# Optimization experiments

Measured on AMD Instinct MI355X. Metric: run time of the kernel, lower is better.

The kernel has to match this reference:

```python
import jax, jax.numpy as jnp
import numpy as np

B, NX, NY, NZ = 2, 64, 64, 64
D, CI, CO, F = 3, 32, 32, 64  # spatial dims, chan in/out, n_modes


def setup_inputs() -> dict:
    key = jax.random.key(0)
    ka, kx, ky, k1, k2, k3, k4, k5, k6 = jax.random.split(key, 9)
    omega, c = 30.0 / 300.0, 6.0
    u = lambda k, shape, scale: scale * (2.0 * jax.random.uniform(k, shape, jnp.float32) - 1.0)
    return {
        "a": jax.random.normal(ka, (B, NX, NY, NZ, CI), jnp.float32),
        "x": jax.random.uniform(kx, (B, NX, NY, NZ, D), jnp.float32),
        "y": jax.random.uniform(ky, (B, NX, NY, NZ, D), jnp.float32),
        "modes_a": u(k1, (F, CI), np.sqrt(c / (CI + F))),
        "modes_x": u(k2, (F, D), np.sqrt(c / (D + F)) * omega),
        "modes_y": u(k3, (F, D), np.sqrt(c / (D + F)) * omega),
        "modes_u": u(k4, (F, CO), np.sqrt(c / (F + CO))),
        "fc_w": jax.random.normal(k5, (CI, CO), jnp.float32) / np.sqrt(CI),
        "fc_b": jax.random.normal(k6, (CO,), jnp.float32) * 0.01,
    }


def reference(a, x, y, modes_a, modes_x, modes_y, modes_u, fc_w, fc_b):
    # SpectralAttention: Fourier-feature linear attention.
    # NOTE: source forward passes x for both coordinate args (att(h, x, x)).
    A = jnp.einsum('bxyzi,fi->bxyzf', a, modes_a)                       # [B,NX,NY,NZ,F]
    X = jnp.exp(-2j * np.pi * jnp.einsum('bxyzd,gd->bxyzg', x, modes_x))  # complex64
    Y = jnp.exp(2j * np.pi * jnp.einsum('bxyzd,gd->bxyzg', x, modes_y))   # complex64
    N = x.shape[1] * x.shape[2] * x.shape[3]
    AX = jnp.einsum('bxyzf,bxyzg->bfg', A.astype(X.dtype), X)           # [B,F,F] complex
    U = jnp.einsum('bfg,bxyzg->bxyzf', AX, Y).real / N                  # [B,NX,NY,NZ,F]
    u = jnp.einsum('bxyzf,fo->bxyzo', U, modes_u)                        # [B,NX,NY,NZ,CO]
    h = u + a @ fc_w + fc_b                                              # residual Linear
    return jax.nn.gelu(h)
```

## Files before the change

kernel.cpp:

```cpp
#include <hip/hip_runtime.h>
#include <math.h>

#define NB   2
#define NPTS 262144

typedef __attribute__((ext_vector_type(8))) __bf16 bf16x8;
typedef __attribute__((ext_vector_type(4))) float  f32x4;

__device__ __forceinline__ float gelu_tanh(float v) {
    float v3 = v * v * v;
    float z  = 0.7978845608028654f * (v + 0.044715f * v3);
    float e  = __expf(2.0f * z);
    float th = 1.0f - 2.0f / (e + 1.0f);
    return 0.5f * v * (1.0f + th);
}

__device__ __forceinline__ unsigned short bf16_rn(float f) {
    unsigned u = __builtin_bit_cast(unsigned, f);
    u += 0x7fffu + ((u >> 16) & 1u);
    return (unsigned short)(u >> 16);
}

__global__ __launch_bounds__(256)
void pass1_kernel(const float* __restrict__ a, const float* __restrict__ x,
                  const float* __restrict__ mx, float* __restrict__ part, int NPB)
{
    __shared__ float4 xs[4][32];
    __shared__ float wsum[32 * 129];

    const int t = threadIdx.x, wave = t >> 6, lane = t & 63;
    const int l15 = lane & 15, l4 = lane >> 4;
    const int blk = blockIdx.x, b = blk / NPB, pb = blk % NPB;
    const int ppb = NPTS / NPB;
    const int chunks = ppb >> 5;
    const long base = (long)b * NPTS + (long)pb * ppb;

    float m0[4], m1[4], m2[4];
    #pragma unroll
    for (int ct = 0; ct < 4; ++ct) {
        int g = l15 + 16 * ct;
        m0[ct] = mx[g*3]; m1[ct] = mx[g*3+1]; m2[ct] = mx[g*3+2];
    }

    f32x4 acc[2][8];
    #pragma unroll
    for (int rt = 0; rt < 2; ++rt)
        #pragma unroll
        for (int ct = 0; ct < 8; ++ct)
            acc[rt][ct] = f32x4{0.f, 0.f, 0.f, 0.f};

    for (int ci = wave; ci < chunks; ci += 4) {
        const long p0 = base + ((long)ci << 5);
        if (lane < 32) {
            const float* xq = x + (p0 + lane) * 3;
            xs[wave][lane] = make_float4(xq[0], xq[1], xq[2], 0.f);
        }
        float areg[2][8];
        #pragma unroll
        for (int rt = 0; rt < 2; ++rt)
            #pragma unroll
            for (int j = 0; j < 8; ++j)
                areg[rt][j] = a[(p0 + l4*8 + j) * 32 + l15 + 16*rt];
        bf16x8 afr[2];
        #pragma unroll
        for (int rt = 0; rt < 2; ++rt)
            #pragma unroll
            for (int j = 0; j < 8; ++j)
                afr[rt][j] = (__bf16)areg[rt][j];

        float4 xp[8];
        #pragma unroll
        for (int j = 0; j < 8; ++j) xp[j] = xs[wave][l4*8 + j];

        #pragma unroll
        for (int ct = 0; ct < 4; ++ct) {
            bf16x8 bc, bs;
            #pragma unroll
            for (int j = 0; j < 8; ++j) {
                float d = xp[j].x*m0[ct] + xp[j].y*m1[ct] + xp[j].z*m2[ct];
                bc[j] = (__bf16)__builtin_amdgcn_cosf(d);
                bs[j] = (__bf16)__builtin_amdgcn_sinf(d);
            }
            #pragma unroll
            for (int rt = 0; rt < 2; ++rt) {
                acc[rt][ct]   = __builtin_amdgcn_mfma_f32_16x16x32_bf16(afr[rt], bc, acc[rt][ct],   0, 0, 0);
                acc[rt][ct+4] = __builtin_amdgcn_mfma_f32_16x16x32_bf16(afr[rt], bs, acc[rt][ct+4], 0, 0, 0);
            }
        }
    }

    for (int w = 0; w < 4; ++w) {
        if (wave == w) {
            #pragma unroll
            for (int rt = 0; rt < 2; ++rt)
                #pragma unroll
                for (int ct = 0; ct < 8; ++ct)
                    #pragma unroll
                    for (int r = 0; r < 4; ++r) {
                        int i = 16*rt + l4*4 + r;
                        int c = ((ct & 3) * 16) + l15 + ((ct & 4) ? 64 : 0);
                        int id = i * 129 + c;
                        float v = acc[rt][ct][r];
                        if (w == 0) wsum[id] = v; else wsum[id] += v;
                    }
        }
        __syncthreads();
    }
    for (int idx = t; idx < 4096; idx += 256) {
        int i = idx >> 7, c = idx & 127;
        part[(long)blk * 4096 + idx] = wsum[i * 129 + c];
    }
}

__global__ __launch_bounds__(256)
void reduceW_kernel(const float* __restrict__ part, float* __restrict__ Wf, int NPB)
{
    __shared__ float red[8][33];
    const int t = threadIdx.x;
    const int b = blockIdx.x >> 7;
    const int jb = (blockIdx.x & 127) * 32;
    const int jj = jb + (t & 31), seg = t >> 5;
    const float* p = part + (long)b * NPB * 4096 + jj;
    float s = 0.f;
    for (int pb = seg; pb < NPB; pb += 8) s += p[(long)pb * 4096];
    red[seg][t & 31] = s;
    __syncthreads();
    if (t < 32) {
        float r = 0.f;
        #pragma unroll
        for (int q = 0; q < 8; ++q) r += red[q][t];
        Wf[b * 4096 + jb + t] = r;
    }
}

__global__ __launch_bounds__(256)
void vmat_kernel(const float* __restrict__ Wf, const float* __restrict__ ma,
                 const float* __restrict__ mu, const float* __restrict__ fcw,
                 unsigned short* __restrict__ Vb)
{
    __shared__ float Ws[4096];
    __shared__ float Mas[64 * 32], Mus[64 * 32];
    __shared__ float Qs[32][32];
    const int t = threadIdx.x, b = blockIdx.x;

    for (int i = t; i < 4096; i += 256) Ws[i] = Wf[b * 4096 + i];
    for (int i = t; i < 2048; i += 256) { Mas[i] = ma[i]; Mus[i] = mu[i]; }
    __syncthreads();
    for (int i = t; i < 1024; i += 256) {
        int o = i >> 5, ii = i & 31;
        float s = 0.f;
        for (int f = 0; f < 64; ++f) s += Mus[f*32 + o] * Mas[f*32 + ii];
        Qs[o][ii] = s;
    }
    __syncthreads();
    const float invN = 1.f / 262144.f;
    for (int i = t; i < 5120; i += 256) {
        int k = i >> 5, o = i & 31;
        float v;
        if (k < 128) {
            int g = k & 63, off = (k >= 64) ? 64 : 0;
            float s = 0.f;
            for (int q = 0; q < 32; ++q) s += Qs[o][q] * Ws[q*128 + off + g];
            v = s * invN;
        } else {
            v = fcw[(k - 128) * 32 + o];
        }
        Vb[b * 5120 + i] = bf16_rn(v);
    }
}

__global__ __launch_bounds__(256)
void pass2_kernel(const float* __restrict__ a, const float* __restrict__ x,
                  const unsigned short* __restrict__ Vb, const float* __restrict__ fcb,
                  const float* __restrict__ my, float* __restrict__ out)
{
    __shared__ float4 xs[4][32];
    __shared__ float4 mys[64];
    const int t = threadIdx.x, wave = t >> 6, lane = t & 63;
    const int l15 = lane & 15, l4 = lane >> 4;
    const int blk = blockIdx.x, b = blk >> 9, lb = blk & 511;
    const long base = (long)b * NPTS + (long)lb * 512;

    if (t < 64) { const float* mq = my + t*3; mys[t] = make_float4(mq[0], mq[1], mq[2], 0.f); }

    bf16x8 bfr[5][2];
    {
        const unsigned short* vb = Vb + b * 5120;
        #pragma unroll
        for (int c = 0; c < 5; ++c)
            #pragma unroll
            for (int ct = 0; ct < 2; ++ct) {
                bf16x8 tmp;
                #pragma unroll
                for (int j = 0; j < 8; ++j) {
                    unsigned short uv = vb[(32*c + l4*8 + j) * 32 + l15 + 16*ct];
                    tmp[j] = __builtin_bit_cast(__bf16, uv);
                }
                bfr[c][ct] = tmp;
            }
    }
    const float bias0 = fcb[l15], bias1 = fcb[l15 + 16];
    __syncthreads();

    for (int ci = wave; ci < 16; ci += 4) {
        const long p0 = base + ((long)ci << 5);
        if (lane < 32) {
            const float* xq = x + (p0 + lane) * 3;
            xs[wave][lane] = make_float4(xq[0], xq[1], xq[2], 0.f);
        }
        bf16x8 afr[2];
        #pragma unroll
        for (int rt = 0; rt < 2; ++rt) {
            const float* ap = a + (p0 + l15 + 16*rt) * 32 + l4*8;
            float4 a0 = *(const float4*)ap;
            float4 a1 = *(const float4*)(ap + 4);
            afr[rt][0] = (__bf16)a0.x; afr[rt][1] = (__bf16)a0.y;
            afr[rt][2] = (__bf16)a0.z; afr[rt][3] = (__bf16)a0.w;
            afr[rt][4] = (__bf16)a1.x; afr[rt][5] = (__bf16)a1.y;
            afr[rt][6] = (__bf16)a1.z; afr[rt][7] = (__bf16)a1.w;
        }
        float4 xp0 = xs[wave][l15];
        float4 xp1 = xs[wave][l15 + 16];
        bf16x8 ac[2][2], as_[2][2];
        #pragma unroll
        for (int j = 0; j < 8; ++j) {
            float4 mA = mys[l4*8 + j];
            float4 mB = mys[32 + l4*8 + j];
            float dA0 = xp0.x*mA.x + xp0.y*mA.y + xp0.z*mA.z;
            float dB0 = xp0.x*mB.x + xp0.y*mB.y + xp0.z*mB.z;
            float dA1 = xp1.x*mA.x + xp1.y*mA.y + xp1.z*mA.z;
            float dB1 = xp1.x*mB.x + xp1.y*mB.y + xp1.z*mB.z;
            ac[0][0][j]  = (__bf16)__builtin_amdgcn_cosf(dA0);
            as_[0][0][j] = (__bf16)__builtin_amdgcn_sinf(dA0);
            ac[0][1][j]  = (__bf16)__builtin_amdgcn_cosf(dB0);
            as_[0][1][j] = (__bf16)__builtin_amdgcn_sinf(dB0);
            ac[1][0][j]  = (__bf16)__builtin_amdgcn_cosf(dA1);
            as_[1][0][j] = (__bf16)__builtin_amdgcn_sinf(dA1);
            ac[1][1][j]  = (__bf16)__builtin_amdgcn_cosf(dB1);
            as_[1][1][j] = (__bf16)__builtin_amdgcn_sinf(dB1);
        }
        #pragma unroll
        for (int rt = 0; rt < 2; ++rt)
            #pragma unroll
            for (int ct = 0; ct < 2; ++ct) {
                f32x4 acc = f32x4{0.f, 0.f, 0.f, 0.f};
                acc = __builtin_amdgcn_mfma_f32_16x16x32_bf16(ac[rt][0],  bfr[0][ct], acc, 0, 0, 0);
                acc = __builtin_amdgcn_mfma_f32_16x16x32_bf16(ac[rt][1],  bfr[1][ct], acc, 0, 0, 0);
                acc = __builtin_amdgcn_mfma_f32_16x16x32_bf16(as_[rt][0], bfr[2][ct], acc, 0, 0, 0);
                acc = __builtin_amdgcn_mfma_f32_16x16x32_bf16(as_[rt][1], bfr[3][ct], acc, 0, 0, 0);
                acc = __builtin_amdgcn_mfma_f32_16x16x32_bf16(afr[rt],    bfr[4][ct], acc, 0, 0, 0);
                float bias = ct ? bias1 : bias0;
                #pragma unroll
                for (int r = 0; r < 4; ++r) {
                    long p = p0 + 16*rt + l4*4 + r;
                    out[p * 32 + l15 + 16*ct] = gelu_tanh(acc[r] + bias);
                }
            }
    }
}

extern "C" void kernel_launch(void* const* d_in, const int* in_sizes, int n_in,
                              void* d_out, int out_size, void* d_ws, size_t ws_size,
                              hipStream_t stream)
{
    const float* a   = (const float*)d_in[0];
    const float* x   = (const float*)d_in[1];
    const float* ma  = (const float*)d_in[3];
    const float* mx  = (const float*)d_in[4];
    const float* my  = (const float*)d_in[5];
    const float* mu  = (const float*)d_in[6];
    const float* fcw = (const float*)d_in[7];
    const float* fcb = (const float*)d_in[8];
    float* out = (float*)d_out;

    int NPB = 256;
    while (NPB > 32) {
        size_t need = (size_t)NB * NPB * 4096 * 4 + (size_t)NB * 4096 * 4
                    + (size_t)NB * 5120 * 2 + 256;
        if (need <= ws_size) break;
        NPB >>= 1;
    }
    float* part = (float*)d_ws;
    float* Wf = part + (size_t)NB * NPB * 4096;
    unsigned short* Vb = (unsigned short*)(Wf + NB * 4096);

    pass1_kernel<<<NB * NPB, 256, 0, stream>>>(a, x, mx, part, NPB);
    reduceW_kernel<<<NB * 128, 256, 0, stream>>>(part, Wf, NPB);
    vmat_kernel<<<NB, 256, 0, stream>>>(Wf, ma, mu, fcw, Vb);
    pass2_kernel<<<NB * 512, 256, 0, stream>>>(a, x, Vb, fcb, my, out);
}
```

Measured before the change: 86.25 us.

## Vectorize pass1 a loads, restructure pass2 MFMA loop, cheaper GELU, more partitions

In pass1, each lane now reads a float2 of adjacent channels instead of 16 scalar strided loads, and the reduction row index is remapped to match the permuted channel assignment. In pass2, the cos/sin feature tiles are generated per mode-half and fed straight into persistent accumulators, which lowers peak register use. GELU becomes an exp2/rcp sigmoid form of the tanh approximation. The pass1 partition count is doubled, giving more blocks but a larger partial-sum buffer for reduceW to reduce.

After: 90.83 us. 1.05x slower.

```diff
diff --git a/kernel.cpp b/kernel.cpp
--- a/kernel.cpp
+++ b/kernel.cpp
@@ -7,12 +7,11 @@
 typedef __attribute__((ext_vector_type(8))) __bf16 bf16x8;
 typedef __attribute__((ext_vector_type(4))) float  f32x4;
 
-__device__ __forceinline__ float gelu_tanh(float v) {
-    float v3 = v * v * v;
-    float z  = 0.7978845608028654f * (v + 0.044715f * v3);
-    float e  = __expf(2.0f * z);
-    float th = 1.0f - 2.0f / (e + 1.0f);
-    return 0.5f * v * (1.0f + th);
+__device__ __forceinline__ float gelu_fast(float v) {
+    float t  = v * v;
+    float z2 = v * (-2.302208f + -0.1029432f * t);
+    float e  = __builtin_amdgcn_exp2f(z2);
+    return v * __builtin_amdgcn_rcpf(1.0f + e);
 }
 
 __device__ __forceinline__ unsigned short bf16_rn(float f) {
@@ -55,18 +54,13 @@
             const float* xq = x + (p0 + lane) * 3;
             xs[wave][lane] = make_float4(xq[0], xq[1], xq[2], 0.f);
         }
-        float areg[2][8];
-        #pragma unroll
-        for (int rt = 0; rt < 2; ++rt)
-            #pragma unroll
-            for (int j = 0; j < 8; ++j)
-                areg[rt][j] = a[(p0 + l4*8 + j) * 32 + l15 + 16*rt];
         bf16x8 afr[2];
         #pragma unroll
-        for (int rt = 0; rt < 2; ++rt)
-            #pragma unroll
-            for (int j = 0; j < 8; ++j)
-                afr[rt][j] = (__bf16)areg[rt][j];
+        for (int j = 0; j < 8; ++j) {
+            float2 av = *(const float2*)(a + (p0 + l4*8 + j) * 32 + 2*l15);
+            afr[0][j] = (__bf16)av.x;
+            afr[1][j] = (__bf16)av.y;
+        }
 
         float4 xp[8];
         #pragma unroll
@@ -97,7 +91,7 @@
                 for (int ct = 0; ct < 8; ++ct)
                     #pragma unroll
                     for (int r = 0; r < 4; ++r) {
-                        int i = 16*rt + l4*4 + r;
+                        int i = 2 * (l4*4 + r) + rt;
                         int c = ((ct & 3) * 16) + l15 + ((ct & 4) ? 64 : 0);
                         int id = i * 129 + c;
                         float v = acc[rt][ct][r];
@@ -221,39 +215,45 @@
         }
         float4 xp0 = xs[wave][l15];
         float4 xp1 = xs[wave][l15 + 16];
-        bf16x8 ac[2][2], as_[2][2];
-        #pragma unroll
-        for (int j = 0; j < 8; ++j) {
-            float4 mA = mys[l4*8 + j];
-            float4 mB = mys[32 + l4*8 + j];
-            float dA0 = xp0.x*mA.x + xp0.y*mA.y + xp0.z*mA.z;
-            float dB0 = xp0.x*mB.x + xp0.y*mB.y + xp0.z*mB.z;
-            float dA1 = xp1.x*mA.x + xp1.y*mA.y + xp1.z*mA.z;
-            float dB1 = xp1.x*mB.x + xp1.y*mB.y + xp1.z*mB.z;
-            ac[0][0][j]  = (__bf16)__builtin_amdgcn_cosf(dA0);
-            as_[0][0][j] = (__bf16)__builtin_amdgcn_sinf(dA0);
-            ac[0][1][j]  = (__bf16)__builtin_amdgcn_cosf(dB0);
-            as_[0][1][j] = (__bf16)__builtin_amdgcn_sinf(dB0);
-            ac[1][0][j]  = (__bf16)__builtin_amdgcn_cosf(dA1);
-            as_[1][0][j] = (__bf16)__builtin_amdgcn_sinf(dA1);
-            ac[1][1][j]  = (__bf16)__builtin_amdgcn_cosf(dB1);
-            as_[1][1][j] = (__bf16)__builtin_amdgcn_sinf(dB1);
-        }
+
+        f32x4 acc[2][2];
         #pragma unroll
         for (int rt = 0; rt < 2; ++rt)
             #pragma unroll
+            for (int ct = 0; ct < 2; ++ct)
+                acc[rt][ct] = f32x4{0.f, 0.f, 0.f, 0.f};
+
+        #pragma unroll
+        for (int gt = 0; gt < 2; ++gt) {
+            bf16x8 ac[2], as2[2];
+            #pragma unroll
+            for (int j = 0; j < 8; ++j) {
+                float4 m = mys[gt*32 + l4*8 + j];
+                float d0 = xp0.x*m.x + xp0.y*m.y + xp0.z*m.z;
+                float d1 = xp1.x*m.x + xp1.y*m.y + xp1.z*m.z;
+                ac[0][j]  = (__bf16)__builtin_amdgcn_cosf(d0);
+                as2[0][j] = (__bf16)__builtin_amdgcn_sinf(d0);
+                ac[1][j]  = (__bf16)__builtin_amdgcn_cosf(d1);
+                as2[1][j] = (__bf16)__builtin_amdgcn_sinf(d1);
+            }
+            #pragma unroll
+            for (int rt = 0; rt < 2; ++rt)
+                #pragma unroll
+                for (int ct = 0; ct < 2; ++ct) {
+                    acc[rt][ct] = __builtin_amdgcn_mfma_f32_16x16x32_bf16(ac[rt],  bfr[gt][ct],   acc[rt][ct], 0, 0, 0);
+                    acc[rt][ct] = __builtin_amdgcn_mfma_f32_16x16x32_bf16(as2[rt], bfr[2+gt][ct], acc[rt][ct], 0, 0, 0);
+                }
+        }
+        #pragma unroll
+        for (int rt = 0; rt < 2; ++rt)
+            #pragma unroll
             for (int ct = 0; ct < 2; ++ct) {
-                f32x4 acc = f32x4{0.f, 0.f, 0.f, 0.f};
-                acc = __builtin_amdgcn_mfma_f32_16x16x32_bf16(ac[rt][0],  bfr[0][ct], acc, 0, 0, 0);
-                acc = __builtin_amdgcn_mfma_f32_16x16x32_bf16(ac[rt][1],  bfr[1][ct], acc, 0, 0, 0);
-                acc = __builtin_amdgcn_mfma_f32_16x16x32_bf16(as_[rt][0], bfr[2][ct], acc, 0, 0, 0);
-                acc = __builtin_amdgcn_mfma_f32_16x16x32_bf16(as_[rt][1], bfr[3][ct], acc, 0, 0, 0);
-                acc = __builtin_amdgcn_mfma_f32_16x16x32_bf16(afr[rt],    bfr[4][ct], acc, 0, 0, 0);
+                acc[rt][ct] = __builtin_amdgcn_mfma_f32_16x16x32_bf16(afr[rt], bfr[4][ct], acc[rt][ct], 0, 0, 0);
                 float bias = ct ? bias1 : bias0;
                 #pragma unroll
                 for (int r = 0; r < 4; ++r) {
                     long p = p0 + 16*rt + l4*4 + r;
-                    out[p * 32 + l15 + 16*ct] = gelu_tanh(acc[r] + bias);
+                    out[p * 32 + l15 + 16*ct] = gelu_fast(acc[rt][ct][r] + bias);
                 }
             }
     }
@@ -273,7 +273,7 @@
     const float* fcb = (const float*)d_in[8];
     float* out = (float*)d_out;
 
-    int NPB = 256;
+    int NPB = 512;
     while (NPB > 32) {
         size_t need = (size_t)NB * NPB * 4096 * 4 + (size_t)NB * 4096 * 4
                     + (size_t)NB * 5120 * 2 + 256;
```
